# Performance work log

Hardware: AMD Instinct MI355X
Metric: run time of the kernel (lower is better)

## Reference

```python
import jax, jax.numpy as jnp
import numpy as np

D_MODEL = 1024
D_STATE = 16
D_CONV = 4
EXPAND = 2
D_INNER = D_MODEL * EXPAND


def setup_inputs() -> dict:
    key = jax.random.key(0)
    ks = jax.random.split(key, 10)
    B, L = 2, 2048
    x = jax.random.normal(ks[0], (B, L, D_MODEL), jnp.float32)
    W_in = jax.random.normal(ks[1], (2 * D_INNER, D_MODEL), jnp.float32) * (1.0 / np.sqrt(D_MODEL))
    conv_w = jax.random.normal(ks[2], (D_INNER, 1, D_CONV), jnp.float32) * (1.0 / np.sqrt(D_CONV))
    conv_b = jax.random.normal(ks[3], (D_INNER,), jnp.float32) * 0.1
    W_x = jax.random.normal(ks[4], (2 * D_STATE + 1, D_INNER), jnp.float32) * (1.0 / np.sqrt(D_INNER))
    A_log = jnp.log(jnp.abs(jax.random.normal(ks[5], (D_INNER, D_STATE), jnp.float32)) + 1e-4)
    D_param = jnp.ones((D_INNER,), jnp.float32)
    W_dt = jax.random.normal(ks[6], (D_INNER, 1), jnp.float32)
    b_dt = jax.random.normal(ks[7], (D_INNER,), jnp.float32) * 0.1
    W_out = jax.random.normal(ks[8], (D_MODEL, D_INNER), jnp.float32) * (1.0 / np.sqrt(D_INNER))
    return {"x": x, "W_in": W_in, "conv_w": conv_w, "conv_b": conv_b, "W_x": W_x,
            "A_log": A_log, "D_param": D_param, "W_dt": W_dt, "b_dt": b_dt, "W_out": W_out}


def _forward(x, W_in, conv_w, conv_b, W_x, A_log, D_param, W_dt, b_dt, W_out):
    B, L, _ = x.shape
    xz = x @ W_in.T                                  # [B,L,2*d_inner]
    x_ssm, z = jnp.split(xz, 2, axis=-1)
    # causal depthwise conv: torch pads both sides d_conv-1 then truncates to L == left-pad only
    xc = jnp.transpose(x_ssm, (0, 2, 1))             # [B,d_inner,L]
    xc = jax.lax.conv_general_dilated(
        xc, conv_w, window_strides=(1,), padding=[(D_CONV - 1, 0)],
        feature_group_count=D_INNER, dimension_numbers=("NCH", "OIH", "NCH"))
    xc = xc + conv_b[None, :, None]
    x_ssm = jax.nn.silu(jnp.transpose(xc, (0, 2, 1)))  # [B,L,d_inner]
    proj = x_ssm @ W_x.T                              # [B,L,2*d_state+1]
    B_ssm = proj[..., :D_STATE]                       # [B,L,d_state]
    C_ssm = proj[..., D_STATE:2 * D_STATE]            # [B,L,d_state]
    dt = jax.nn.softplus(proj[..., -1:] * W_dt[:, 0] + b_dt)  # [B,L,d_inner]
    A = -jnp.exp(A_log)                               # [d_inner,d_state]

    def step(h, inp):
        dt_t, Bt, Ct, xt = inp                        # [B,d_inner],[B,n],[B,n],[B,d_inner]
        dA = jnp.exp(dt_t[..., None] * A)             # [B,d_inner,d_state]
        h = dA * h + (xt * dt_t)[..., None] * Bt[:, None, :]
        y = jnp.einsum("bdn,bn->bd", h, Ct)
        return h, y

    h0 = jnp.zeros((B, D_INNER, D_STATE), x.dtype)
    inputs = (jnp.transpose(dt, (1, 0, 2)), jnp.transpose(B_ssm, (1, 0, 2)),
              jnp.transpose(C_ssm, (1, 0, 2)), jnp.transpose(x_ssm, (1, 0, 2)))
    _, ys = jax.lax.scan(step, h0, inputs)            # ys: [L,B,d_inner]
    y = jnp.transpose(ys, (1, 0, 2)) + x_ssm * D_param
    y = y * jax.nn.silu(z)
    return y @ W_out.T


def reference(x, W_in, conv_w, conv_b, W_x, A_log, D_param, W_dt, b_dt, W_out):
    return _forward(x, W_in, conv_w, conv_b, W_x, A_log, D_param, W_dt, b_dt, W_out)
```

## Files before the change

kernel.cpp:

```cpp
#include <hip/hip_runtime.h>
#include <hip/hip_bf16.h>
#include <cstddef>

#define DMODEL 1024
#define DI     2048
#define DS     16
#define LSEQ   2048
#define BATCH  2
#define NC     128
#define TCH    (LSEQ / NC)

typedef __attribute__((ext_vector_type(8))) short short8;
typedef __attribute__((ext_vector_type(4))) float f32x4;
typedef __attribute__((ext_vector_type(2))) float f32x2;
typedef __attribute__((ext_vector_type(8))) unsigned short us8;

__device__ __forceinline__ unsigned short f2bf(float f) {
    unsigned int u = __float_as_uint(f);
    unsigned int r = (u + 0x7fff + ((u >> 16) & 1)) >> 16;
    return (unsigned short)r;
}
__device__ __forceinline__ float bf2f(unsigned short b) {
    return __uint_as_float(((unsigned int)b) << 16);
}

__device__ __forceinline__ float fexp2(float x) {
#if __has_builtin(__builtin_amdgcn_exp2f)
    return __builtin_amdgcn_exp2f(x);
#else
    return exp2f(x);
#endif
}
__device__ __forceinline__ float flog2(float x) {
#if __has_builtin(__builtin_amdgcn_logf)
    return __builtin_amdgcn_logf(x);
#else
    return log2f(x);
#endif
}

#define LOG2E 1.4426950408889634f
#define RLOG2E 0.6931471805599453f

__device__ __forceinline__ float softplus_f(float v) {
    return (v > 20.f) ? v : flog2(1.f + fexp2(v * LOG2E)) * RLOG2E;
}

__device__ __forceinline__ void gload_lds16(const void* g, void* l) {
    __builtin_amdgcn_global_load_lds(
        (const __attribute__((address_space(1))) unsigned int*)g,
        (__attribute__((address_space(3))) unsigned int*)l, 16, 0, 0);
}

__device__ __forceinline__ void cvt8_store(const float* __restrict__ in,
                                           unsigned short* __restrict__ out, int i) {
    const float4* p = reinterpret_cast<const float4*>(in) + (size_t)i * 2;
    float4 v0 = p[0], v1 = p[1];
    us8 o;
    o[0] = f2bf(v0.x); o[1] = f2bf(v0.y); o[2] = f2bf(v0.z); o[3] = f2bf(v0.w);
    o[4] = f2bf(v1.x); o[5] = f2bf(v1.y); o[6] = f2bf(v1.z); o[7] = f2bf(v1.w);
    *reinterpret_cast<us8*>(out + (size_t)i * 8) = o;
}

#define PREP_X   524288
#define PREP_WI  (PREP_X + 524288)
#define PREP_WO  (PREP_WI + 262144)
#define PREP_WX  (PREP_WO + 12288)
#define PREP_A   (PREP_WX + 32768)
__global__ void prep_all(const float* __restrict__ x, const float* __restrict__ W_in,
                         const float* __restrict__ W_out, const float* __restrict__ wx,
                         const float* __restrict__ A_log,
                         unsigned short* __restrict__ Xb, unsigned short* __restrict__ W_inb,
                         unsigned short* __restrict__ W_outb, unsigned short* __restrict__ Wxb48,
                         float* __restrict__ At2) {
    int i = blockIdx.x * 256 + threadIdx.x;
    if (i < PREP_X) {
        cvt8_store(x, Xb, i);
    } else if (i < PREP_WI) {
        cvt8_store(W_in, W_inb, i - PREP_X);
    } else if (i < PREP_WO) {
        cvt8_store(W_out, W_outb, i - PREP_WI);
    } else if (i < PREP_WX) {
        int j = i - PREP_WO;
        size_t o = (size_t)j * 8;
        int row = (int)(o >> 11);
        if (row < 33) cvt8_store(wx, Wxb48, j);
        else *reinterpret_cast<us8*>(Wxb48 + o) = (us8)0;
    } else if (i < PREP_A) {
        int j = i - PREP_WX;
        int n = j / DI, d = j % DI;
        At2[j] = -__expf(A_log[d * DS + n]) * LOG2E;
    }
}

#define NTK1 32
__global__ __launch_bounds__(512, 4)
void gemm1_2b(const unsigned short* __restrict__ A, const unsigned short* __restrict__ B,
              unsigned short* __restrict__ C) {
    __shared__ unsigned short As[2][128 * 32];
    __shared__ unsigned short Bs[2][256 * 32];

    const int tid = threadIdx.x;
    const int wid = tid >> 6, ln = tid & 63;
    const int wm = wid >> 2, wn = wid & 3;

    int wg = blockIdx.x;
    wg = (wg & 7) * 64 + (wg >> 3);
    const int m0 = (wg >> 4) * 128;
    const int n0 = (wg & 15) * 256;

    const int srow = tid >> 2;
    const int sun  = tid & 3;
    const int ksrc = ((sun ^ ((srow >> 1) & 3)) * 8);

    const int fr = ln & 15;
    const int fku = (ln >> 4);

    f32x4 acc[4][4] = {};

    #define STAGE1(kt, c)                                                                  \
        do {                                                                               \
            gload_lds16(A + (size_t)(m0 + srow) * 1024 + (kt) * 32 + ksrc,                 \
                        &As[c][srow * 32 + sun * 8]);                                      \
            gload_lds16(B + (size_t)(n0 + srow) * 1024 + (kt) * 32 + ksrc,                 \
                        &Bs[c][srow * 32 + sun * 8]);                                      \
            gload_lds16(B + (size_t)(n0 + 128 + srow) * 1024 + (kt) * 32 + ksrc,           \
                        &Bs[c][(128 + srow) * 32 + sun * 8]);                              \
        } while (0)

    STAGE1(0, 0);
    asm volatile("s_waitcnt vmcnt(0)" ::: "memory");
    __builtin_amdgcn_s_barrier();
    __builtin_amdgcn_sched_barrier(0);

    for (int kt = 0; kt < NTK1; ++kt) {
        const int c = kt & 1;
        if (kt + 1 < NTK1) STAGE1(kt + 1, c ^ 1);

        short8 af[4], bfr[4];
        #pragma unroll
        for (int i = 0; i < 4; ++i) {
            int r = wm * 64 + i * 16 + fr;
            int u = fku ^ ((r >> 1) & 3);
            af[i] = *reinterpret_cast<const short8*>(&As[c][r * 32 + u * 8]);
        }
        #pragma unroll
        for (int j = 0; j < 4; ++j) {
            int r = wn * 64 + j * 16 + fr;
            int u = fku ^ ((r >> 1) & 3);
            bfr[j] = *reinterpret_cast<const short8*>(&Bs[c][r * 32 + u * 8]);
        }
        __builtin_amdgcn_sched_barrier(0);
        __builtin_amdgcn_s_setprio(1);
        #pragma unroll
        for (int i = 0; i < 4; ++i)
            #pragma unroll
            for (int j = 0; j < 4; ++j)
                acc[i][j] = __builtin_amdgcn_mfma_f32_16x16x32_bf16(af[i], bfr[j], acc[i][j], 0, 0, 0);
        __builtin_amdgcn_s_setprio(0);
        __builtin_amdgcn_sched_barrier(0);

        if (kt + 1 < NTK1) asm volatile("s_waitcnt vmcnt(0)" ::: "memory");
        __builtin_amdgcn_s_barrier();
        __builtin_amdgcn_sched_barrier(0);
    }
    #undef STAGE1

    const int cr = (ln >> 4) * 4, cc = ln & 15;
    #pragma unroll
    for (int i = 0; i < 4; ++i) {
        int row = m0 + wm * 64 + i * 16 + cr;
        #pragma unroll
        for (int j = 0; j < 4; ++j) {
            int col = n0 + wn * 64 + j * 16 + cc;
            #pragma unroll
            for (int r = 0; r < 4; ++r)
                C[(size_t)(row + r) * 4096 + col] = f2bf(acc[i][j][r]);
        }
    }
}

#define NT3 64
__global__ __launch_bounds__(256, 2)
void gemm3_pipe(const unsigned short* __restrict__ A,
                const unsigned short* __restrict__ B,
                float* __restrict__ C) {
    __shared__ unsigned short As[4][128 * 32];
    __shared__ unsigned short Bs[4][64 * 32];

    const int tid = threadIdx.x;
    const int wid = tid >> 6, ln = tid & 63;
    const int wm = wid >> 1, wn = wid & 1;

    int wg = blockIdx.x;
    wg = (wg & 7) * 64 + (wg >> 3);
    const int m0 = (wg >> 4) * 128;
    const int n0 = (wg & 15) * 64;

    const int srow = tid >> 2;
    const int sun  = tid & 3;
    const int ksrc = ((sun ^ ((srow >> 1) & 3)) * 8);

    const int fr = ln & 15;
    const int fku = (ln >> 4);

    f32x4 acc[4][2] = {};

    #define STAGE3(kt)                                                                     \
        do {                                                                               \
            const int bq_ = (kt) & 3;                                                      \
            gload_lds16(A + (size_t)(m0 + srow) * 2048 + (kt) * 32 + ksrc,                 \
                        &As[bq_][srow * 32 + sun * 8]);                                    \
            gload_lds16(A + (size_t)(m0 + 64 + srow) * 2048 + (kt) * 32 + ksrc,            \
                        &As[bq_][(64 + srow) * 32 + sun * 8]);                             \
            gload_lds16(B + (size_t)(n0 + srow) * 2048 + (kt) * 32 + ksrc,                 \
                        &Bs[bq_][srow * 32 + sun * 8]);                                    \
        } while (0)

    STAGE3(0); STAGE3(1); STAGE3(2);
    asm volatile("s_waitcnt vmcnt(6)" ::: "memory");
    __builtin_amdgcn_s_barrier();
    __builtin_amdgcn_sched_barrier(0);

    for (int kt = 0; kt < NT3; ++kt) {
        const int bq = kt & 3;
        if (kt + 3 < NT3) STAGE3(kt + 3);

        short8 af[4], bfr[2];
        #pragma unroll
        for (int i = 0; i < 4; ++i) {
            int r = wm * 64 + i * 16 + fr;
            int u = fku ^ ((r >> 1) & 3);
            af[i] = *reinterpret_cast<const short8*>(&As[bq][r * 32 + u * 8]);
        }
        #pragma unroll
        for (int j = 0; j < 2; ++j) {
            int r = wn * 32 + j * 16 + fr;
            int u = fku ^ ((r >> 1) & 3);
            bfr[j] = *reinterpret_cast<const short8*>(&Bs[bq][r * 32 + u * 8]);
        }
        __builtin_amdgcn_sched_barrier(0);
        __builtin_amdgcn_s_setprio(1);
        #pragma unroll
        for (int i = 0; i < 4; ++i)
            #pragma unroll
            for (int j = 0; j < 2; ++j)
                acc[i][j] = __builtin_amdgcn_mfma_f32_16x16x32_bf16(af[i], bfr[j], acc[i][j], 0, 0, 0);
        __builtin_amdgcn_s_setprio(0);
        __builtin_amdgcn_sched_barrier(0);

        if (kt < NT3 - 3)       asm volatile("s_waitcnt vmcnt(6)" ::: "memory");
        else if (kt == NT3 - 3) asm volatile("s_waitcnt vmcnt(3)" ::: "memory");
        else if (kt == NT3 - 2) asm volatile("s_waitcnt vmcnt(0)" ::: "memory");
        __builtin_amdgcn_s_barrier();
        __builtin_amdgcn_sched_barrier(0);
    }
    #undef STAGE3

    const int cr = (ln >> 4) * 4, cc = ln & 15;
    #pragma unroll
    for (int i = 0; i < 4; ++i) {
        int row = m0 + wm * 64 + i * 16 + cr;
        #pragma unroll
        for (int j = 0; j < 2; ++j) {
            int col = n0 + wn * 32 + j * 16 + cc;
            #pragma unroll
            for (int r = 0; r < 4; ++r)
                C[(size_t)(row + r) * 1024 + col] = acc[i][j][r];
        }
    }
}

#define RAWS 40
__global__ __launch_bounds__(256)
void gemm_proj_conv(const unsigned short* __restrict__ XZb, const unsigned short* __restrict__ Wxb,
                    const float* __restrict__ cw, const float* __restrict__ cb,
                    float* __restrict__ projp, unsigned short* __restrict__ xactb) {
    __shared__ unsigned short raw[67 * RAWS];
    __shared__ unsigned short Bs[48 * 32];

    const int tid = threadIdx.x;
    const int wv = tid >> 6, ln = tid & 63;
    const int m0 = blockIdx.x * 64;
    const int kz = blockIdx.y;
    const int srow = tid >> 2, skoff = (tid & 3) * 8;
    const int fr = ln & 15;
    const int lhat = wv * 16 + fr;
    const int d0 = (ln >> 4) * 8;

    const bool mstart = ((m0 & 2047) == 0);
    const int colbase = kz * 512;

    f32x4 acc[3] = {};

    for (int k0 = 0; k0 < 512; k0 += 32) {
        for (int j = tid; j < 268; j += 256) {
            int i = j >> 2, slot = j & 3;
            us8 v;
            if (mstart && i < 3) {
                v = (us8)0;
            } else {
                v = *reinterpret_cast<const us8*>(
                    XZb + (size_t)(m0 - 3 + i) * 4096 + colbase + k0 + slot * 8);
            }
            *reinterpret_cast<us8*>(&raw[i * RAWS + slot * 8]) = v;
        }
        if (wv < 3)
            gload_lds16(Wxb + (size_t)srow * 2048 + colbase + k0 + skoff, &Bs[wv * 512]);
        __syncthreads();

        short8 af;
        us8 ax;
        #pragma unroll
        for (int e = 0; e < 8; ++e) {
            int dg = colbase + k0 + d0 + e;
            float a = cb[dg];
            float4 w = *reinterpret_cast<const float4*>(cw + dg * 4);
            a += bf2f(raw[(lhat + 0) * RAWS + d0 + e]) * w.x;
            a += bf2f(raw[(lhat + 1) * RAWS + d0 + e]) * w.y;
            a += bf2f(raw[(lhat + 2) * RAWS + d0 + e]) * w.z;
            a += bf2f(raw[(lhat + 3) * RAWS + d0 + e]) * w.w;
            float v = a / (1.f + __expf(-a));
            unsigned short bfv = f2bf(v);
            ((unsigned short*)&af)[e] = (short)bfv;
            ax[e] = bfv;
        }
        *reinterpret_cast<us8*>(xactb + (size_t)(m0 + lhat) * 2048 + colbase + k0 + d0) = ax;

        #pragma unroll
        for (int j = 0; j < 3; ++j) {
            short8 bf_ = *reinterpret_cast<const short8*>(&Bs[(j * 16 + fr) * 32 + d0]);
            acc[j] = __builtin_amdgcn_mfma_f32_16x16x32_bf16(af, bf_, acc[j], 0, 0, 0);
        }
        __syncthreads();
    }

    const int cr = (ln >> 4) * 4, cc = ln & 15;
    #pragma unroll
    for (int j = 0; j < 3; ++j) {
        int col = j * 16 + cc;
        if (col < 33) {
            #pragma unroll
            for (int r = 0; r < 4; ++r) {
                int row = m0 + wv * 16 + cr + r;
                projp[(size_t)row * 144 + kz * 36 + col] = acc[j][r];
            }
        }
    }
}

__global__ __launch_bounds__(256)
void scan_phase1(const unsigned short* __restrict__ xactb, const float* __restrict__ projp,
                 const float* __restrict__ At2, const float* __restrict__ W_dt,
                 const float* __restrict__ b_dt, const float* __restrict__ Dp,
                 unsigned short* __restrict__ Hend,
                 float* __restrict__ dtsum, unsigned short* __restrict__ yloc) {
    __shared__ float prS[TCH][34];

    const int d = blockIdx.x * 256 + threadIdx.x;
    const int c = blockIdx.y;
    const int b = blockIdx.z;
    const size_t r0 = (size_t)(b * LSEQ + c * TCH);

    for (int idx = threadIdx.x; idx < TCH * 33; idx += 256) {
        int rl = idx / 33, col = idx % 33;
        const float* pp = projp + (r0 + rl) * 144 + col;
        prS[rl][col] = ((pp[0] + pp[36]) + pp[72]) + pp[108];
    }
    __syncthreads();

    f32x2 A2[DS / 2], h2[DS / 2];
    #pragma unroll
    for (int p = 0; p < DS / 2; ++p) {
        A2[p] = (f32x2){At2[(2 * p) * DI + d], At2[(2 * p + 1) * DI + d]};
        h2[p] = (f32x2){0.f, 0.f};
    }
    const float wdt = W_dt[d], bdt = b_dt[d], Dv = Dp[d];
    float ssum = 0.f;

    #pragma unroll 2
    for (int rl = 0; rl < TCH; ++rl) {
        const size_t row = r0 + rl;
        const float* pr = prS[rl];
        float dt = softplus_f(pr[32] * wdt + bdt);
        ssum += dt;
        float x = bf2f(xactb[row * DI + d]);
        float xdt = x * dt;
        f32x2 xdt2 = (f32x2){xdt, xdt};
        f32x2 y2 = (f32x2){0.f, 0.f};
        #pragma unroll
        for (int p = 0; p < DS / 2; ++p) {
            f32x2 t = A2[p] * dt;
            f32x2 e2 = (f32x2){fexp2(t.x), fexp2(t.y)};
            h2[p] = e2 * h2[p] + xdt2 * (f32x2){pr[2 * p], pr[2 * p + 1]};
            y2 += h2[p] * (f32x2){pr[16 + 2 * p], pr[17 + 2 * p]};
        }
        yloc[row * DI + d] = f2bf(y2.x + y2.y + x * Dv);
    }
    size_t base = ((size_t)(b * NC + c) * DS) * DI + d;
    #pragma unroll
    for (int p = 0; p < DS / 2; ++p) {
        Hend[base + (size_t)(2 * p) * DI]     = f2bf(h2[p].x);
        Hend[base + (size_t)(2 * p + 1) * DI] = f2bf(h2[p].y);
    }
    dtsum[(size_t)(b * NC + c) * DI + d] = ssum;
}

__global__ void scan_phase2(unsigned short* __restrict__ H, const float* __restrict__ dtsum,
                            const float* __restrict__ At2) {
    int idx = blockIdx.x * 256 + threadIdx.x;
    int b = idx / (DS * DI);
    int r = idx % (DS * DI);
    int n = r / DI, d = r % DI;
    float A2 = At2[n * DI + d];
    float h = 0.f;
    #pragma unroll 4
    for (int c = 0; c < NC; ++c) {
        size_t off = ((size_t)(b * NC + c) * DS + n) * DI + d;
        float He = bf2f(H[off]);
        float P = fexp2(A2 * dtsum[(size_t)(b * NC + c) * DI + d]);
        H[off] = f2bf(h);
        h = P * h + He;
    }
}

__global__ __launch_bounds__(256)
void scan_phase3(const unsigned short* __restrict__ yloc,
                 const float* __restrict__ projp, const float* __restrict__ At2,
                 const float* __restrict__ W_dt, const float* __restrict__ b_dt,
                 const unsigned short* __restrict__ Hin,
                 const unsigned short* __restrict__ XZb,
                 unsigned short* __restrict__ YB2) {
    __shared__ float prS[TCH][34];

    const int tid = threadIdx.x;
    const int d = blockIdx.x * 256 + tid;
    const int c = blockIdx.y;
    const int b = blockIdx.z;
    const size_t r0 = (size_t)(b * LSEQ + c * TCH);

    for (int idx = tid; idx < TCH * 33; idx += 256) {
        int rl = idx / 33, col = idx % 33;
        const float* pp = projp + (r0 + rl) * 144 + col;
        prS[rl][col] = ((pp[0] + pp[36]) + pp[72]) + pp[108];
    }
    __syncthreads();

    f32x2 A2[DS / 2], Hn2[DS / 2];
    size_t hbase = ((size_t)(b * NC + c) * DS) * DI + d;
    #pragma unroll
    for (int p = 0; p < DS / 2; ++p) {
        A2[p]  = (f32x2){At2[(2 * p) * DI + d], At2[(2 * p + 1) * DI + d]};
        Hn2[p] = (f32x2){bf2f(Hin[hbase + (size_t)(2 * p) * DI]),
                         bf2f(Hin[hbase + (size_t)(2 * p + 1) * DI])};
    }
    const float wdt = W_dt[d], bdt = b_dt[d];
    float S = 0.f;

    #pragma unroll 2
    for (int rl = 0; rl < TCH; ++rl) {
        const size_t row = r0 + rl;
        const float* pr = prS[rl];
        float dt = softplus_f(pr[32] * wdt + bdt);
        S += dt;
        float yl = bf2f(yloc[row * DI + d]);
        float z  = bf2f(XZb[row * 4096 + 2048 + d]);
        f32x2 corr2 = (f32x2){0.f, 0.f};
        #pragma unroll
        for (int p = 0; p < DS / 2; ++p) {
            f32x2 t = A2[p] * S;
            f32x2 e2 = (f32x2){fexp2(t.x), fexp2(t.y)};
            corr2 += (f32x2){pr[16 + 2 * p], pr[17 + 2 * p]} * e2 * Hn2[p];
        }
        float y = yl + corr2.x + corr2.y;
        float sz = z / (1.f + __expf(-z));
        YB2[row * DI + d] = f2bf(y * sz);
    }
}

extern "C" void kernel_launch(void* const* d_in, const int* in_sizes, int n_in,
                              void* d_out, int out_size, void* d_ws, size_t ws_size,
                              hipStream_t stream) {
    const float* x      = (const float*)d_in[0];
    const float* W_in   = (const float*)d_in[1];
    const float* conv_w = (const float*)d_in[2];
    const float* conv_b = (const float*)d_in[3];
    const float* W_x    = (const float*)d_in[4];
    const float* A_log  = (const float*)d_in[5];
    const float* Dp     = (const float*)d_in[6];
    const float* W_dt   = (const float*)d_in[7];
    const float* b_dt   = (const float*)d_in[8];
    const float* W_out  = (const float*)d_in[9];
    float* out = (float*)d_out;

    char* ws = (char*)d_ws;
    unsigned short* XZb   = (unsigned short*)(ws + 0);
    unsigned short* XACTB = (unsigned short*)(ws + 33554432);
    unsigned short* Xb    = (unsigned short*)(ws + 50331648);
    unsigned short* W_inb = (unsigned short*)(ws + 58720256);
    unsigned short* YB2   = (unsigned short*)(ws + 50331648);
    unsigned short* Hbuf  = (unsigned short*)(ws + 67108864);
    unsigned short* YLOC  = (unsigned short*)(ws + 83886080);
    float* DTSUM = (float*)(ws + 101711872);
    float* PROJP = (float*)(ws + 103809024);
    float* Abuf  = (float*)(ws + 106954752);
    unsigned short* W_outb = (unsigned short*)(ws + 108003328);
    unsigned short* Wxb48  = (unsigned short*)(ws + 112197632);

    const int M = BATCH * LSEQ;

    prep_all<<<(PREP_A + 255) / 256, 256, 0, stream>>>(
        x, W_in, W_out, W_x, A_log, Xb, W_inb, W_outb, Wxb48, Abuf);

    gemm1_2b<<<512, 512, 0, stream>>>(Xb, W_inb, XZb);

    gemm_proj_conv<<<dim3(M / 64, 4), 256, 0, stream>>>(
        XZb, Wxb48, conv_w, conv_b, PROJP, XACTB);

    scan_phase1<<<dim3(DI / 256, NC, BATCH), 256, 0, stream>>>(
        XACTB, PROJP, Abuf, W_dt, b_dt, Dp, Hbuf, DTSUM, YLOC);
    scan_phase2<<<BATCH * DS * DI / 256, 256, 0, stream>>>(Hbuf, DTSUM, Abuf);
    scan_phase3<<<dim3(DI / 256, NC, BATCH), 256, 0, stream>>>(
        YLOC, PROJP, Abuf, W_dt, b_dt, Hbuf, XZb, YB2);

    gemm3_pipe<<<512, 256, 0, stream>>>(YB2, W_outb, out);
}
```

Baseline: 194.1 us.

## Recompute conv+silu in scan phase1 instead of storing activations; widen proj split-K

The projection GEMM no longer writes the bf16 conv-activated x buffer. Scan phase1 instead recomputes the causal depthwise conv and SiLU from XZb, using a three-row sliding register window. The projection split-K grows from 4 to 16 slices for more blocks, and a new proj_combine kernel reduces the partials once so the scan kernels read a combined proj array directly rather than summing partials into shared memory. This trades a 16 MB write and read of activations for extra conv arithmetic, one extra launch, and a larger partial buffer.

```diff
diff --git a/kernel.cpp b/kernel.cpp
--- a/kernel.cpp
+++ b/kernel.cpp
@@ -275,7 +275,7 @@
 __global__ __launch_bounds__(256)
 void gemm_proj_conv(const unsigned short* __restrict__ XZb, const unsigned short* __restrict__ Wxb,
                     const float* __restrict__ cw, const float* __restrict__ cb,
-                    float* __restrict__ projp, unsigned short* __restrict__ xactb) {
+                    float* __restrict__ projp) {
     __shared__ unsigned short raw[67 * RAWS];
     __shared__ unsigned short Bs[48 * 32];
 
@@ -289,11 +289,11 @@
     const int d0 = (ln >> 4) * 8;
 
     const bool mstart = ((m0 & 2047) == 0);
-    const int colbase = kz * 512;
+    const int colbase = kz * 128;
 
     f32x4 acc[3] = {};
 
-    for (int k0 = 0; k0 < 512; k0 += 32) {
+    for (int k0 = 0; k0 < 128; k0 += 32) {
         for (int j = tid; j < 268; j += 256) {
             int i = j >> 2, slot = j & 3;
             us8 v;
@@ -310,7 +310,6 @@
         __syncthreads();
 
         short8 af;
-        us8 ax;
         #pragma unroll
         for (int e = 0; e < 8; ++e) {
             int dg = colbase + k0 + d0 + e;
@@ -321,11 +320,8 @@
             a += bf2f(raw[(lhat + 2) * RAWS + d0 + e]) * w.z;
             a += bf2f(raw[(lhat + 3) * RAWS + d0 + e]) * w.w;
             float v = a / (1.f + __expf(-a));
-            unsigned short bfv = f2bf(v);
-            ((unsigned short*)&af)[e] = (short)bfv;
-            ax[e] = bfv;
-        }
-        *reinterpret_cast<us8*>(xactb + (size_t)(m0 + lhat) * 2048 + colbase + k0 + d0) = ax;
+            ((unsigned short*)&af)[e] = (short)f2bf(v);
+        }
 
         #pragma unroll
         for (int j = 0; j < 3; ++j) {
@@ -343,32 +339,36 @@
             #pragma unroll
             for (int r = 0; r < 4; ++r) {
                 int row = m0 + wv * 16 + cr + r;
-                projp[(size_t)row * 144 + kz * 36 + col] = acc[j][r];
+                projp[(size_t)row * 576 + kz * 36 + col] = acc[j][r];
             }
         }
     }
 }
 
+__global__ void proj_combine(const float* __restrict__ projp, float* __restrict__ proj) {
+    int idx = blockIdx.x * 256 + threadIdx.x;
+    if (idx >= BATCH * LSEQ * 33) return;
+    int row = idx / 33, col = idx % 33;
+    const float* pp = projp + (size_t)row * 576 + col;
+    float s = 0.f;
+    #pragma unroll
+    for (int kz = 0; kz < 16; ++kz)
+        s += pp[kz * 36];
+    proj[(size_t)row * 36 + col] = s;
+}
+
 __global__ __launch_bounds__(256)
-void scan_phase1(const unsigned short* __restrict__ xactb, const float* __restrict__ projp,
+void scan_phase1(const unsigned short* __restrict__ XZb, const float* __restrict__ proj,
                  const float* __restrict__ At2, const float* __restrict__ W_dt,
                  const float* __restrict__ b_dt, const float* __restrict__ Dp,
+                 const float* __restrict__ cw, const float* __restrict__ cb,
                  unsigned short* __restrict__ Hend,
                  float* __restrict__ dtsum, unsigned short* __restrict__ yloc) {
-    __shared__ float prS[TCH][34];
-
     const int d = blockIdx.x * 256 + threadIdx.x;
     const int c = blockIdx.y;
     const int b = blockIdx.z;
     const size_t r0 = (size_t)(b * LSEQ + c * TCH);
 
-    for (int idx = threadIdx.x; idx < TCH * 33; idx += 256) {
-        int rl = idx / 33, col = idx % 33;
-        const float* pp = projp + (r0 + rl) * 144 + col;
-        prS[rl][col] = ((pp[0] + pp[36]) + pp[72]) + pp[108];
-    }
-    __syncthreads();
-
     f32x2 A2[DS / 2], h2[DS / 2];
     #pragma unroll
     for (int p = 0; p < DS / 2; ++p) {
@@ -376,15 +376,30 @@
         h2[p] = (f32x2){0.f, 0.f};
     }
     const float wdt = W_dt[d], bdt = b_dt[d], Dv = Dp[d];
+    const float4 w = *reinterpret_cast<const float4*>(cw + d * 4);
+    const float cbv = cb[d];
+
+    float r3, r2, r1;
+    if (c == 0) {
+        r3 = r2 = r1 = 0.f;
+    } else {
+        r3 = bf2f(XZb[(r0 - 3) * 4096 + d]);
+        r2 = bf2f(XZb[(r0 - 2) * 4096 + d]);
+        r1 = bf2f(XZb[(r0 - 1) * 4096 + d]);
+    }
     float ssum = 0.f;
 
     #pragma unroll 2
     for (int rl = 0; rl < TCH; ++rl) {
         const size_t row = r0 + rl;
-        const float* pr = prS[rl];
+        const float* pr = proj + row * 36;
         float dt = softplus_f(pr[32] * wdt + bdt);
         ssum += dt;
-        float x = bf2f(xactb[row * DI + d]);
+        float rr = bf2f(XZb[row * 4096 + d]);
+        float a = cbv + r3 * w.x + r2 * w.y + r1 * w.z + rr * w.w;
+        r3 = r2; r2 = r1; r1 = rr;
+        float v = a / (1.f + __expf(-a));
+        float x = bf2f(f2bf(v));
         float xdt = x * dt;
         f32x2 xdt2 = (f32x2){xdt, xdt};
         f32x2 y2 = (f32x2){0.f, 0.f};
@@ -426,26 +441,17 @@
 
 __global__ __launch_bounds__(256)
 void scan_phase3(const unsigned short* __restrict__ yloc,
-                 const float* __restrict__ projp, const float* __restrict__ At2,
+                 const float* __restrict__ proj, const float* __restrict__ At2,
                  const float* __restrict__ W_dt, const float* __restrict__ b_dt,
                  const unsigned short* __restrict__ Hin,
                  const unsigned short* __restrict__ XZb,
                  unsigned short* __restrict__ YB2) {
-    __shared__ float prS[TCH][34];
-
     const int tid = threadIdx.x;
     const int d = blockIdx.x * 256 + tid;
     const int c = blockIdx.y;
     const int b = blockIdx.z;
     const size_t r0 = (size_t)(b * LSEQ + c * TCH);
 
-    for (int idx = tid; idx < TCH * 33; idx += 256) {
-        int rl = idx / 33, col = idx % 33;
-        const float* pp = projp + (r0 + rl) * 144 + col;
-        prS[rl][col] = ((pp[0] + pp[36]) + pp[72]) + pp[108];
-    }
-    __syncthreads();
-
     f32x2 A2[DS / 2], Hn2[DS / 2];
     size_t hbase = ((size_t)(b * NC + c) * DS) * DI + d;
     #pragma unroll
@@ -460,7 +466,7 @@
     #pragma unroll 2
     for (int rl = 0; rl < TCH; ++rl) {
         const size_t row = r0 + rl;
-        const float* pr = prS[rl];
+        const float* pr = proj + row * 36;
         float dt = softplus_f(pr[32] * wdt + bdt);
         S += dt;
         float yl = bf2f(yloc[row * DI + d]);
@@ -495,14 +501,14 @@
 
     char* ws = (char*)d_ws;
     unsigned short* XZb   = (unsigned short*)(ws + 0);
-    unsigned short* XACTB = (unsigned short*)(ws + 33554432);
+    float* PROJP = (float*)(ws + 33554432);
     unsigned short* Xb    = (unsigned short*)(ws + 50331648);
     unsigned short* W_inb = (unsigned short*)(ws + 58720256);
     unsigned short* YB2   = (unsigned short*)(ws + 50331648);
     unsigned short* Hbuf  = (unsigned short*)(ws + 67108864);
     unsigned short* YLOC  = (unsigned short*)(ws + 83886080);
+    float* PROJ  = (float*)(ws + 100663296);
     float* DTSUM = (float*)(ws + 101711872);
-    float* PROJP = (float*)(ws + 103809024);
     float* Abuf  = (float*)(ws + 106954752);
     unsigned short* W_outb = (unsigned short*)(ws + 108003328);
     unsigned short* Wxb48  = (unsigned short*)(ws + 112197632);
@@ -514,14 +520,15 @@
 
     gemm1_2b<<<512, 512, 0, stream>>>(Xb, W_inb, XZb);
 
-    gemm_proj_conv<<<dim3(M / 64, 4), 256, 0, stream>>>(
-        XZb, Wxb48, conv_w, conv_b, PROJP, XACTB);
+    gemm_proj_conv<<<dim3(M / 64, 16), 256, 0, stream>>>(
+        XZb, Wxb48, conv_w, conv_b, PROJP);
+    proj_combine<<<(M * 33 + 255) / 256, 256, 0, stream>>>(PROJP, PROJ);
 
     scan_phase1<<<dim3(DI / 256, NC, BATCH), 256, 0, stream>>>(
-        XACTB, PROJP, Abuf, W_dt, b_dt, Dp, Hbuf, DTSUM, YLOC);
+        XZb, PROJ, Abuf, W_dt, b_dt, Dp, conv_w, conv_b, Hbuf, DTSUM, YLOC);
     scan_phase2<<<BATCH * DS * DI / 256, 256, 0, stream>>>(Hbuf, DTSUM, Abuf);
     scan_phase3<<<dim3(DI / 256, NC, BATCH), 256, 0, stream>>>(
-        YLOC, PROJP, Abuf, W_dt, b_dt, Hbuf, XZb, YB2);
+        YLOC, PROJ, Abuf, W_dt, b_dt, Hbuf, XZb, YB2);
 
     gemm3_pipe<<<512, 256, 0, stream>>>(YB2, W_outb, out);
 }
```

New measurement: 182.7 us (median of 3 runs). 1.06x faster.
